# Optimization experiments

Measured on AMD Instinct MI355X. Metric: run time of the kernel, lower is better.

Reference implementation:

```python
import jax, jax.numpy as jnp
import numpy as np

GRID = 64
DX = 1.0 / GRID            # grid spacing (buffer dx)
RADIUS = 2.5 * DX          # search_radius = dx * 2.5
CIN, COUT = 16, 16
B, N = 2, 8192
EPS = 1e-12
FOUR_OVER_PI = 4.0 / np.pi


def _safe_sqrt(v):
    return jnp.sqrt(jnp.maximum(v, EPS))


def _sphere_to_cylinder(x, y, z):
    # volume-preserving map: unit ball -> cylinder (radius 1, height 2)
    sq = x * x + y * y + z * z
    norm = _safe_sqrt(sq)
    xy2 = x * x + y * y
    cap = 1.25 * z * z > xy2                      # polar-cap region
    s_cap = jnp.sqrt(3.0 * norm / (norm + jnp.abs(z) + EPS))
    s_side = norm / _safe_sqrt(xy2)
    xc = jnp.where(cap, x * s_cap, x * s_side)
    yc = jnp.where(cap, y * s_cap, y * s_side)
    zc = jnp.where(cap, jnp.sign(z) * norm, 1.5 * z)
    zero = sq <= EPS
    z0 = jnp.zeros_like(x)
    return (jnp.where(zero, z0, xc), jnp.where(zero, z0, yc), jnp.where(zero, z0, zc))


def _cylinder_to_cube(x, y, z):
    # area-preserving disc -> square on the xy cross-section
    xy2 = x * x + y * y
    nxy = _safe_sqrt(xy2)
    xdom = jnp.abs(y) <= jnp.abs(x)
    safe_x = jnp.where(jnp.abs(x) > EPS, x, 1.0)
    safe_y = jnp.where(jnp.abs(y) > EPS, y, 1.0)
    tx = jnp.sign(x) * nxy
    ty = jnp.sign(y) * nxy
    xa, ya = tx, tx * FOUR_OVER_PI * jnp.arctan(y / safe_x)
    xb, yb = ty * FOUR_OVER_PI * jnp.arctan(x / safe_y), ty
    xc = jnp.where(xdom, xa, xb)
    yc = jnp.where(xdom, ya, yb)
    zero = xy2 <= EPS
    z0 = jnp.zeros_like(x)
    return jnp.where(zero, z0, xc), jnp.where(zero, z0, yc), z


def _cconv_forward(input, pos, weights, grid_pos):
    Bb, C, D, H, Wd = input.shape
    Np = pos.shape[1]
    # [B,C,D,H,W] -> [B,D,H,W,C] -> [B,G,C]  (matches permute+view in torch)
    feat = jnp.transpose(input, (0, 2, 3, 4, 1)).reshape(Bb, D * H * Wd, C)
    # fixed 6^3 stencil of candidate grid cells around each point
    off = jnp.arange(6) - 2
    o0, o1, o2 = jnp.meshgrid(off, off, off, indexing='ij')
    offs = jnp.stack([o0, o1, o2], axis=-1).reshape(-1, 3)          # [216,3]
    base = jnp.floor(pos / DX).astype(jnp.int32)                    # [B,N,3]
    cand = base[:, :, None, :] + offs[None, None]                   # [B,N,216,3]
    dims = jnp.array([D, H, Wd])
    in_bounds = jnp.all((cand >= 0) & (cand < dims), axis=-1)       # [B,N,216]
    cc = jnp.clip(cand, 0, dims - 1)
    flat = (cc[..., 0] * H + cc[..., 1]) * Wd + cc[..., 2]          # [B,N,216]
    bidx = jnp.arange(Bb)[:, None, None]
    npos = grid_pos[flat]                                           # [B,N,216,3]
    fg = feat[bidx, flat]                                           # [B,N,216,C]
    rel = npos - pos[:, :, None, :]
    dist2 = jnp.sum(rel * rel, axis=-1)
    valid = in_bounds & (dist2 <= RADIUS * RADIUS)
    # map relative offsets (scaled to the unit ball) to the unit cube
    u = rel / RADIUS
    x, y, z = _sphere_to_cylinder(u[..., 0], u[..., 1], u[..., 2])
    x, y, z = _cylinder_to_cube(x, y, z)
    # linear interpolation of the 3x3x3 kernel, align_corners=True -> coords in [0,2]
    taps = jnp.arange(3, dtype=pos.dtype)
    def hat(c):
        c = jnp.clip((c * 0.5 + 0.5) * 2.0, 0.0, 2.0)
        return jnp.maximum(0.0, 1.0 - jnp.abs(c[..., None] - taps))  # [B,N,216,3]
    w0, w1, w2 = hat(x), hat(y), hat(z)
    w27 = jnp.einsum('bnki,bnkj,bnkl->bnkijl', w0, w1, w2).reshape(Bb, Np, -1, 27)
    w27 = w27 * valid[..., None].astype(w27.dtype)
    # accumulate interpolated features per kernel tap, then apply the kernel
    acc = jnp.einsum('bnkt,bnkc->bntc', w27, fg)                    # [B,N,27,C]
    out = jnp.einsum('bntc,tcd->bnd', acc, weights.reshape(27, C, -1))
    # normalize=True (Open3D default): divide by neighbor count
    count = jnp.sum(valid, axis=-1).astype(out.dtype)
    out = out / jnp.maximum(count, 1.0)[..., None]
    return out


def setup_inputs() -> dict:
    key = jax.random.key(0)
    k1, k2, k3 = jax.random.split(key, 3)
    inp = jax.random.normal(k1, (B, CIN, GRID, GRID, GRID), jnp.float32)
    pos = jax.random.uniform(k2, (B, N, 3), jnp.float32)
    weights = jax.random.normal(k3, (3, 3, 3, CIN, COUT), jnp.float32) * 0.05
    ax = jnp.arange(GRID, dtype=jnp.float32) * DX
    g = jnp.stack(jnp.meshgrid(ax, ax, ax, indexing='ij'), axis=-1).reshape(-1, 3)
    return {"input": inp, "pos": pos, "weights": weights, "grid_pos": g}


def reference(input, pos, weights, grid_pos):
    return _cconv_forward(input, pos, weights, grid_pos)
```

## Files before the change

kernel.cpp:

```cpp
#include <hip/hip_runtime.h>
#include <cstdint>

typedef float v2f __attribute__((ext_vector_type(2)));

namespace {
constexpr int kG = 262144;
constexpr int kB = 2;
constexpr int kN = 8192;
constexpr int kPts = kB * kN;
constexpr float kDX = 1.0f / 64.0f;
constexpr float kRad2 = 0.00152587890625f;
constexpr float kInvRad = 25.6f;
constexpr float kEps = 1e-12f;
constexpr float kFourOverPi = 1.27323954473516268615f;

constexpr int PPB = 2;
constexpr int THREADS = PPB * 64;
constexpr int MAXREC = 96;
constexpr int SLOT = 12;
constexpr int NFLAT = 96;
constexpr int GSTRIDE = MAXREC * SLOT + NFLAT;
}

__device__ __forceinline__ float sgnf(float v) {
    return (v > 0.f) ? 1.f : ((v < 0.f) ? -1.f : 0.f);
}

__global__ __launch_bounds__(256) void transpose_feat_k(const float* __restrict__ in,
                                                        float* __restrict__ feat) {
    int idx = blockIdx.x * 256 + threadIdx.x;
    if (idx >= kB * kG) return;
    int b = idx >> 18;
    int g = idx & (kG - 1);
    float v[16];
#pragma unroll
    for (int c = 0; c < 16; ++c) v[c] = in[((size_t)(b * 16 + c)) * kG + g];
    float4* dst = reinterpret_cast<float4*>(feat + (size_t)idx * 16);
    dst[0] = make_float4(v[0], v[1], v[2], v[3]);
    dst[1] = make_float4(v[4], v[5], v[6], v[7]);
    dst[2] = make_float4(v[8], v[9], v[10], v[11]);
    dst[3] = make_float4(v[12], v[13], v[14], v[15]);
}

__global__ __launch_bounds__(THREADS) void cconv_main(
    const float* __restrict__ input, const float* __restrict__ pos,
    const float* __restrict__ W, const float* __restrict__ feat,
    float* __restrict__ out, int use_feat)
{
    __shared__ __align__(16) float rec[PPB * GSTRIDE];

    const int tid = threadIdx.x;
    const int wv = tid >> 6;
    const int lane = tid & 63;
    const int sg = lane >> 4;
    const int lig = lane & 15;
    const int pt = blockIdx.x * PPB + wv;
    const int b = pt >> 13;

    const float px = pos[pt * 3 + 0];
    const float py = pos[pt * 3 + 1];
    const float pz = pos[pt * 3 + 2];
    const int bx = (int)floorf(px * 64.f);
    const int by = (int)floorf(py * 64.f);
    const int bz = (int)floorf(pz * 64.f);

    float* grec = rec + wv * GSTRIDE;
    int* iflats = reinterpret_cast<int*>(grec + MAXREC * SLOT);
    int nv = 0;

#pragma unroll
    for (int it = 0; it < 4; ++it) {
        int k = it * 64 + lane;
        bool valid = false;
        float rx = 0.f, ry = 0.f, rz = 0.f;
        int flat16 = 0;
        if (k < 216) {
            int a = k / 36;
            int r = k - a * 36;
            int b1 = r / 6;
            int c1 = r - b1 * 6;
            int g0 = bx + a - 2, g1 = by + b1 - 2, g2 = bz + c1 - 2;
            bool inb = (g0 >= 0) & (g0 < 64) & (g1 >= 0) & (g1 < 64) &
                       (g2 >= 0) & (g2 < 64);
            int q0 = min(max(g0, 0), 63);
            int q1 = min(max(g1, 0), 63);
            int q2 = min(max(g2, 0), 63);
            flat16 = ((q0 * 64 + q1) * 64 + q2) << 4;
            rx = __fsub_rn((float)q0 * kDX, px);
            ry = __fsub_rn((float)q1 * kDX, py);
            rz = __fsub_rn((float)q2 * kDX, pz);
            float d2 = __fadd_rn(__fadd_rn(__fmul_rn(rx, rx), __fmul_rn(ry, ry)),
                                 __fmul_rn(rz, rz));
            valid = inb && (d2 <= kRad2);
        }
        unsigned long long ball = __ballot(valid);
        if (valid) {
            int slot = nv + __popcll(ball & ((1ull << lane) - 1ull));
            *reinterpret_cast<float4*>(grec + slot * SLOT) =
                make_float4(rx, ry, rz, 0.f);
            iflats[slot] = flat16;
        }
        nv += (int)__popcll(ball);
    }
    __builtin_amdgcn_wave_barrier();

    for (int z = nv + lane; z < MAXREC; z += 64) {
        float4 zf = make_float4(0.f, 0.f, 0.f, 0.f);
        float4* zp = reinterpret_cast<float4*>(grec + z * SLOT);
        zp[0] = zf; zp[1] = zf; zp[2] = zf;
        iflats[z] = 0;
    }
    __builtin_amdgcn_wave_barrier();

    const float* fbp = use_feat ? (feat + (size_t)b * kG * 16)
                                : (input + (size_t)b * 16 * kG);
#define LDF(IDX) (use_feat ? fbp[(size_t)iflats[(IDX)] + lig]                 \
                           : fbp[(size_t)lig * kG + (iflats[(IDX)] >> 4)])
    float fa0 = LDF(sg),      fa1 = LDF(sg + 4);
    float fa2 = LDF(sg + 8),  fa3 = LDF(sg + 12);
    float fb0 = LDF(sg + 16), fb1 = LDF(sg + 20);
    float fb2 = LDF(sg + 24), fb3 = LDF(sg + 28);

    for (int s = lane; s < nv; s += 64) {
        float* rp = grec + s * SLOT;
        float4 rc = *reinterpret_cast<const float4*>(rp);
        float ux = rc.x * kInvRad, uy = rc.y * kInvRad, uz = rc.z * kInvRad;

        float xx = ux * ux, yy = uy * uy, zz = uz * uz;
        float xy2 = xx + yy;
        float sq = xy2 + zz;
        float nrm = __builtin_amdgcn_sqrtf(fmaxf(sq, kEps));
        bool cap = (1.25f * zz > xy2);
        float scap = __builtin_amdgcn_sqrtf(3.f * nrm) *
                     __builtin_amdgcn_rsqf(nrm + fabsf(uz) + kEps);
        float sside = nrm * __builtin_amdgcn_rsqf(fmaxf(xy2, kEps));
        float sc = cap ? scap : sside;
        float xc = ux * sc, yc = uy * sc;
        float zc = cap ? sgnf(uz) * nrm : 1.5f * uz;
        if (sq <= kEps) { xc = 0.f; yc = 0.f; zc = 0.f; }

        float xy2b = xc * xc + yc * yc;
        float nxy = __builtin_amdgcn_sqrtf(fmaxf(xy2b, kEps));
        bool xdom = (fabsf(yc) <= fabsf(xc));
        float num = xdom ? yc : xc;
        float den = xdom ? xc : yc;
        float dsafe = (fabsf(den) > kEps) ? den : 1.0f;
        float r = num * __builtin_amdgcn_rcpf(dsafe);
        float r2 = r * r;
        float at = -0.01172120f;
        at = at * r2 + 0.05265332f;
        at = at * r2 - 0.11643287f;
        at = at * r2 + 0.19354346f;
        at = at * r2 - 0.33262347f;
        at = at * r2 + 0.99997726f;
        at = at * r;
        float tt = sgnf(den) * nxy;
        float g = tt * kFourOverPi * at;
        float xo = xdom ? tt : g;
        float yo = xdom ? g : tt;
        if (xy2b <= kEps) { xo = 0.f; yo = 0.f; }
        float zo = zc;

        float tx = fminf(fmaxf(xo + 1.f, 0.f), 2.f) - 1.f;
        float ty = fminf(fmaxf(yo + 1.f, 0.f), 2.f) - 1.f;
        float tz = fminf(fmaxf(zo + 1.f, 0.f), 2.f) - 1.f;
        float wx0 = fmaxf(0.f, -tx), wx1 = 1.f - fabsf(tx), wx2 = fmaxf(0.f, tx);
        float wy0 = fmaxf(0.f, -ty), wy1 = 1.f - fabsf(ty), wy2 = fmaxf(0.f, ty);
        float wz0 = fmaxf(0.f, -tz), wz1 = 1.f - fabsf(tz);

        float4* rp4 = reinterpret_cast<float4*>(rp);
        rp4[0] = make_float4(wx0 * wy0, wx0 * wy1, wx0 * wy2, wx1 * wy0);
        rp4[1] = make_float4(wx1 * wy1, wx1 * wy2, wx2 * wy0, wx2 * wy1);
        rp4[2] = make_float4(wx2 * wy2, wz0, wz1, 0.f);
    }
    __builtin_amdgcn_wave_barrier();

    v2f az0_01 = {0.f, 0.f}, az1_01 = {0.f, 0.f}, az2_01 = {0.f, 0.f};
    v2f az0_23 = {0.f, 0.f}, az1_23 = {0.f, 0.f}, az2_23 = {0.f, 0.f};
    v2f az0_45 = {0.f, 0.f}, az1_45 = {0.f, 0.f}, az2_45 = {0.f, 0.f};
    v2f az0_67 = {0.f, 0.f}, az1_67 = {0.f, 0.f}, az2_67 = {0.f, 0.f};
    float a8_0 = 0.f, a8_1 = 0.f, a8_2 = 0.f;

    const int R = (nv + 7) & ~7;
    const int F = R >> 4;
    const bool HB = (R & 8) != 0;

#define REC_FMA(S, FV)                                                        \
  {                                                                           \
    const float4* rp4_ = reinterpret_cast<const float4*>(grec + (S) * SLOT);  \
    float4 Wa = rp4_[0], Wb = rp4_[1], Wc = rp4_[2];                          \
    float m0 = Wc.y * (FV), m1 = Wc.z * (FV);                                 \
    float m2 = ((1.f - Wc.y) - Wc.z) * (FV);                                  \
    v2f mz0 = {m0, m0}, mz1 = {m1, m1}, mz2 = {m2, m2};                       \
    v2f p01 = {Wa.x, Wa.y}, p23 = {Wa.z, Wa.w};                               \
    v2f p45 = {Wb.x, Wb.y}, p67 = {Wb.z, Wb.w};                               \
    az0_01 = __builtin_elementwise_fma(p01, mz0, az0_01);                     \
    az1_01 = __builtin_elementwise_fma(p01, mz1, az1_01);                     \
    az2_01 = __builtin_elementwise_fma(p01, mz2, az2_01);                     \
    az0_23 = __builtin_elementwise_fma(p23, mz0, az0_23);                     \
    az1_23 = __builtin_elementwise_fma(p23, mz1, az1_23);                     \
    az2_23 = __builtin_elementwise_fma(p23, mz2, az2_23);                     \
    az0_45 = __builtin_elementwise_fma(p45, mz0, az0_45);                     \
    az1_45 = __builtin_elementwise_fma(p45, mz1, az1_45);                     \
    az2_45 = __builtin_elementwise_fma(p45, mz2, az2_45);                     \
    az0_67 = __builtin_elementwise_fma(p67, mz0, az0_67);                     \
    az1_67 = __builtin_elementwise_fma(p67, mz1, az1_67);                     \
    az2_67 = __builtin_elementwise_fma(p67, mz2, az2_67);                     \
    a8_0 = __builtin_fmaf(Wc.x, m0, a8_0);                                    \
    a8_1 = __builtin_fmaf(Wc.x, m1, a8_1);                                    \
    a8_2 = __builtin_fmaf(Wc.x, m2, a8_2);                                    \
  }

#define P2BODY(KK, F0_, F1_, F2_, F3_)                                        \
  {                                                                           \
    const int rb_ = (KK) * 16 + sg;                                           \
    const bool nxt_ = ((KK) + 2 < F) || ((KK) + 2 == F && HB);                \
    float n0_ = 0.f, n1_ = 0.f, n2_ = 0.f, n3_ = 0.f;                         \
    if (nxt_) {                                                               \
      n0_ = LDF(rb_ + 32); n1_ = LDF(rb_ + 36);                               \
      n2_ = LDF(rb_ + 40); n3_ = LDF(rb_ + 44);                               \
    }                                                                         \
    REC_FMA(rb_, F0_); REC_FMA(rb_ + 4, F1_);                                 \
    if ((KK) < F) { REC_FMA(rb_ + 8, F2_); REC_FMA(rb_ + 12, F3_); }          \
    if (nxt_) { F0_ = n0_; F1_ = n1_; F2_ = n2_; F3_ = n3_; }                 \
  }

     P2BODY(0, fa0, fa1, fa2, fa3)
    if (1 < F || (1 == F && HB)) P2BODY(1, fb0, fb1, fb2, fb3)
    if (2 < F || (2 == F && HB)) P2BODY(2, fa0, fa1, fa2, fa3)
    if (3 < F || (3 == F && HB)) P2BODY(3, fb0, fb1, fb2, fb3)
    if (4 < F || (4 == F && HB)) P2BODY(4, fa0, fa1, fa2, fa3)
    if (5 == F && HB)            P2BODY(5, fb0, fb1, fb2, fb3)

    float acc[28] = {
        az0_01.x, az1_01.x, az2_01.x,
        az0_01.y, az1_01.y, az2_01.y,
        az0_23.x, az1_23.x, az2_23.x,
        az0_23.y, az1_23.y, az2_23.y,
        az0_45.x, az1_45.x, az2_45.x,
        az0_45.y, az1_45.y, az2_45.y,
        az0_67.x, az1_67.x, az2_67.x,
        az0_67.y, az1_67.y, az2_67.y,
        a8_0,     a8_1,     a8_2,
        0.f
    };

    const bool hi32 = (lane >= 32);
    float kp[14];
#pragma unroll
    for (int j = 0; j < 14; ++j) {
        float send = hi32 ? acc[j] : acc[14 + j];
        float recv = __shfl_xor(send, 32);
        kp[j] = (hi32 ? acc[14 + j] : acc[j]) + recv;
    }
    const bool hi16 = (lane & 16) != 0;
    float kk[7];
#pragma unroll
    for (int j = 0; j < 7; ++j) {
        float send = hi16 ? kp[j] : kp[7 + j];
        float recv = __shfl_xor(send, 16);
        kk[j] = (hi16 ? kp[7 + j] : kp[j]) + recv;
    }

    float partial[16];
#pragma unroll
    for (int d = 0; d < 16; ++d) partial[d] = 0.f;
    const float* wbase = W + (sg * 7) * 256 + lig * 16;
#pragma unroll
    for (int j = 0; j < 7; ++j) {
        if (sg * 7 + j < 27) {
            const float4* wr = reinterpret_cast<const float4*>(wbase + j * 256);
            float4 a0 = wr[0], a1 = wr[1], a2 = wr[2], a3 = wr[3];
            float at_ = kk[j];
            partial[0]  += at_ * a0.x; partial[1]  += at_ * a0.y;
            partial[2]  += at_ * a0.z; partial[3]  += at_ * a0.w;
            partial[4]  += at_ * a1.x; partial[5]  += at_ * a1.y;
            partial[6]  += at_ * a1.z; partial[7]  += at_ * a1.w;
            partial[8]  += at_ * a2.x; partial[9]  += at_ * a2.y;
            partial[10] += at_ * a2.z; partial[11] += at_ * a2.w;
            partial[12] += at_ * a3.x; partial[13] += at_ * a3.y;
            partial[14] += at_ * a3.z; partial[15] += at_ * a3.w;
        }
    }

#pragma unroll
    for (int half = 8; half >= 1; half >>= 1) {
        bool up = (lig & half) != 0;
#pragma unroll
        for (int j = 0; j < half; ++j) {
            float send = up ? partial[j] : partial[j + half];
            float recv = __shfl_xor(send, half);
            partial[j] = (up ? partial[j + half] : partial[j]) + recv;
        }
    }
    float res = partial[0];
    res += __shfl_xor(res, 16);
    res += __shfl_xor(res, 32);
    res = res / fmaxf((float)nv, 1.f);
    if (lane < 16) out[(size_t)pt * 16 + lig] = res;
#undef LDF
#undef REC_FMA
#undef P2BODY
}

extern "C" void kernel_launch(void* const* d_in, const int* in_sizes, int n_in,
                              void* d_out, int out_size, void* d_ws, size_t ws_size,
                              hipStream_t stream) {
    const float* input = (const float*)d_in[0];
    const float* pos   = (const float*)d_in[1];
    const float* W     = (const float*)d_in[2];
    float* out  = (float*)d_out;
    float* feat = (float*)d_ws;

    const size_t feat_bytes = (size_t)kB * kG * 16 * sizeof(float);
    int use_feat = (d_ws != nullptr && ws_size >= feat_bytes) ? 1 : 0;

    if (use_feat) {
        transpose_feat_k<<<(kB * kG + 255) / 256, 256, 0, stream>>>(input, feat);
    }
    cconv_main<<<kPts / PPB, THREADS, 0, stream>>>(input, pos, W, feat, out, use_feat);
}
```

Before: 75.07 us.

## Sort points by Morton-ordered spatial bucket to improve gather cache locality

Adds a single-block counting-sort kernel that groups points by a Morton code of their 4-cell spatial bucket, per batch. The main kernel maps each block to points through this order and swizzles block IDs so that concurrently running blocks, spread across XCDs, handle nearby points. The aim is better L2 and MALL reuse of the gathered grid features. In exchange it adds a serial single-block sort launch and an extra indirection, and it only runs when the workspace is large enough.

```diff
diff --git a/kernel.cpp b/kernel.cpp
--- a/kernel.cpp
+++ b/kernel.cpp
@@ -20,10 +20,62 @@
 constexpr int SLOT = 12;
 constexpr int NFLAT = 96;
 constexpr int GSTRIDE = MAXREC * SLOT + NFLAT;
+constexpr int NBUCKET = 8192;
 }
 
 __device__ __forceinline__ float sgnf(float v) {
     return (v > 0.f) ? 1.f : ((v < 0.f) ? -1.f : 0.f);
+}
+
+__global__ __launch_bounds__(1024) void sort_points_k(const float* __restrict__ pos,
+                                                      int* __restrict__ order) {
+    __shared__ int hist[NBUCKET];
+    __shared__ int aux[1024];
+    const int t = threadIdx.x;
+    for (int i = t; i < NBUCKET; i += 1024) hist[i] = 0;
+    __syncthreads();
+
+    int karr[16];
+#pragma unroll
+    for (int j = 0; j < 16; ++j) {
+        int p = j * 1024 + t;
+        float px = pos[p * 3], py = pos[p * 3 + 1], pz = pos[p * 3 + 2];
+        int cx = ((int)floorf(px * 64.f)) >> 2;
+        int cy = ((int)floorf(py * 64.f)) >> 2;
+        int cz = ((int)floorf(pz * 64.f)) >> 2;
+        int rx = (cx & 1) | ((cx & 2) << 2) | ((cx & 4) << 4) | ((cx & 8) << 6);
+        int ry = (cy & 1) | ((cy & 2) << 2) | ((cy & 4) << 4) | ((cy & 8) << 6);
+        int rz = (cz & 1) | ((cz & 2) << 2) | ((cz & 4) << 4) | ((cz & 8) << 6);
+        int key = (rx | (ry << 1) | (rz << 2)) | ((p >> 13) << 12);
+        karr[j] = key;
+        atomicAdd(&hist[key], 1);
+    }
+    __syncthreads();
+
+    const int base = t * 8;
+    int h[8];
+    int s = 0;
+#pragma unroll
+    for (int k = 0; k < 8; ++k) { h[k] = hist[base + k]; s += h[k]; }
+    aux[t] = s;
+    __syncthreads();
+    for (int off = 1; off < 1024; off <<= 1) {
+        int v = (t >= off) ? aux[t - off] : 0;
+        __syncthreads();
+        aux[t] += v;
+        __syncthreads();
+    }
+    int excl = aux[t] - s;
+#pragma unroll
+    for (int k = 0; k < 8; ++k) { hist[base + k] = excl; excl += h[k]; }
+    __syncthreads();
+
+#pragma unroll
+    for (int j = 0; j < 16; ++j) {
+        int p = j * 1024 + t;
+        int idx = atomicAdd(&hist[karr[j]], 1);
+        order[idx] = p;
+    }
 }
 
 __global__ __launch_bounds__(256) void transpose_feat_k(const float* __restrict__ in,
@@ -45,7 +97,8 @@
 __global__ __launch_bounds__(THREADS) void cconv_main(
     const float* __restrict__ input, const float* __restrict__ pos,
     const float* __restrict__ W, const float* __restrict__ feat,
-    float* __restrict__ out, int use_feat)
+    const int* __restrict__ order, float* __restrict__ out,
+    int use_feat, int use_sort)
 {
     __shared__ __align__(16) float rec[PPB * GSTRIDE];
 
@@ -54,7 +107,10 @@
     const int lane = tid & 63;
     const int sg = lane >> 4;
     const int lig = lane & 15;
-    const int pt = blockIdx.x * PPB + wv;
+    const int bid = (int)blockIdx.x;
+    const int swz = use_sort ? ((bid & 7) * 1024 + (bid >> 3)) : bid;
+    const int gid = swz * PPB + wv;
+    const int pt = use_sort ? order[gid] : gid;
     const int b = pt >> 13;
 
     const float px = pos[pt * 3 + 0];
@@ -313,10 +369,17 @@
     float* feat = (float*)d_ws;
 
     const size_t feat_bytes = (size_t)kB * kG * 16 * sizeof(float);
+    const size_t sort_bytes = (size_t)kPts * sizeof(int);
     int use_feat = (d_ws != nullptr && ws_size >= feat_bytes) ? 1 : 0;
-
+    int use_sort = (d_ws != nullptr && ws_size >= feat_bytes + sort_bytes) ? 1 : 0;
+    int* order = (int*)((char*)d_ws + feat_bytes);
+
+    if (use_sort) {
+        sort_points_k<<<1, 1024, 0, stream>>>(pos, order);
+    }
     if (use_feat) {
         transpose_feat_k<<<(kB * kG + 255) / 256, 256, 0, stream>>>(input, feat);
     }
-    cconv_main<<<kPts / PPB, THREADS, 0, stream>>>(input, pos, W, feat, out, use_feat);
-}
+    cconv_main<<<kPts / PPB, THREADS, 0, stream>>>(input, pos, W, feat, order, out,
+                                                   use_feat, use_sort);
+}
```

After: 93.69 us. +24.8%, slower.
